# Optimization experiments

Hardware: AMD Instinct MI355X
Metric: run time of the kernel (lower is better)

The kernel has to match this reference:

```python
import jax, jax.numpy as jnp
import numpy as np

B, S, D, H, DM = 2, 2048, 1024, 16, 4
HD = D // H  # head_dim = 64
EPS = 1e-5


def setup_inputs() -> dict:
    key = jax.random.key(0)
    ks = jax.random.split(key, 8)
    s = 0.02
    return {
        "x": jax.random.normal(ks[0], (B, S, D), jnp.float32),
        "wq": jax.random.normal(ks[1], (D, D), jnp.float32) * s,
        "wk": jax.random.normal(ks[2], (D, D), jnp.float32) * s,
        "wv": jax.random.normal(ks[3], (D, D), jnp.float32) * s,
        "wo": jax.random.normal(ks[4], (D, D), jnp.float32) * s,
        "bo": jnp.zeros((D,), jnp.float32),
        "ln1_scale": jnp.ones((D,), jnp.float32),
        "ln1_shift": jnp.zeros((D,), jnp.float32),
        "ln2_scale": jnp.ones((D,), jnp.float32),
        "ln2_shift": jnp.zeros((D,), jnp.float32),
        "w1": jax.random.normal(ks[5], (DM * D, D), jnp.float32) * s,
        "b1": jnp.zeros((DM * D,), jnp.float32),
        "w2": jax.random.normal(ks[6], (D, DM * D), jnp.float32) * s,
        "b2": jnp.zeros((D,), jnp.float32),
    }


def _layernorm(x, scale, shift):
    mean = jnp.mean(x, axis=-1, keepdims=True)
    var = jnp.var(x, axis=-1, keepdims=True)  # unbiased=False
    return scale * (x - mean) * jax.lax.rsqrt(var + EPS) + shift


def _attn(x, wq, wk, wv, wo, bo):
    b, n, d = x.shape
    # torch Linear: y = x @ W.T
    q = (x @ wq.T).reshape(b, n, H, HD).transpose(0, 2, 1, 3)  # [b,h,n,hd]
    k = (x @ wk.T).reshape(b, n, H, HD).transpose(0, 2, 1, 3)
    v = (x @ wv.T).reshape(b, n, H, HD).transpose(0, 2, 1, 3)
    scores = jnp.einsum("bhqd,bhkd->bhqk", q, k)
    causal = jnp.tril(jnp.ones((n, n), bool))
    scores = jnp.where(causal, scores, -jnp.inf)
    w = jax.nn.softmax(scores / np.sqrt(HD).astype(np.float32), axis=-1)
    ctx = jnp.einsum("bhqk,bhkd->bhqd", w, v)
    ctx = ctx.transpose(0, 2, 1, 3).reshape(b, n, d)
    return ctx @ wo.T + bo


def reference(x, wq, wk, wv, wo, bo, ln1_scale, ln1_shift, ln2_scale, ln2_shift, w1, b1, w2, b2):
    h = x + _attn(_layernorm(x, ln1_scale, ln1_shift), wq, wk, wv, wo, bo)
    y = _layernorm(h, ln2_scale, ln2_shift)
    y = jax.nn.relu(y @ w1.T + b1) @ w2.T + b2
    return h + y
```

## Files before the change

kernel.cpp:

```cpp
#include <hip/hip_runtime.h>
#include <hip/hip_bf16.h>

#define DEV __device__ __forceinline__

typedef __attribute__((ext_vector_type(8))) short bf8;
typedef __attribute__((ext_vector_type(4))) float f4;
typedef __attribute__((ext_vector_type(16))) float f16x;

#define GLOAD_LDS(gp, lp) \
  __builtin_amdgcn_global_load_lds( \
      (const __attribute__((address_space(1))) void*)(gp), \
      (__attribute__((address_space(3))) void*)(lp), 16, 0, 0)

DEV unsigned short f2bf(float f) {
  union { __hip_bfloat16 h; unsigned short u; } c;
  c.h = __float2bfloat16(f);
  return c.u;
}
DEV unsigned int pk2(float a, float b) {
  union { __hip_bfloat162 h; unsigned int u; } c;
  c.h = __hip_bfloat162(__float2bfloat16(a), __float2bfloat16(b));
  return c.u;
}

DEV int2 swz_tile(int ob, int nxt, int nyt) {
  const int nb = nxt * nyt;
  const int cpx = nb >> 3;
  const int W = (ob & 7) * cpx + (ob >> 3);
  const int scw = 4 * nyt;
  const int sc = W / scw, rem = W - sc * scw;
  return make_int2(rem >> 2, sc * 4 + (rem & 3));
}

template<bool BIAS, bool RELU, bool OUTBF>
__global__ __launch_bounds__(512, 2) void gemm_bt256(
    const unsigned short* __restrict__ A, const unsigned short* __restrict__ B,
    const float* __restrict__ bias, void* __restrict__ Cout,
    int M, int N, int K, int ldc, int nyt)
{
  __shared__ unsigned short Sl[2][2][256 * 64];
  const int t = threadIdx.x;
  const int w = t >> 6, l = t & 63;
  const int wr = w >> 2, wc = w & 3;
  int2 tt = swz_tile((int)blockIdx.x, N >> 8, nyt);
  const int m0 = tt.x * 256, n0 = tt.y * 256;

  const int srow = w * 32 + (l >> 3);
  const int scol = 8 * ((l & 7) ^ (l >> 3));
  const unsigned short* Ab = A + (size_t)(m0 + srow) * K + scol;
  const unsigned short* Bb = B + (size_t)(n0 + srow) * K + scol;
  const int sdst = w * 2048 + l * 8;

  auto STAGE = [&](int slot, int kt) {
#pragma unroll
    for (int i = 0; i < 4; ++i) {
      GLOAD_LDS(Ab + (size_t)i * 8 * K + kt * 64, &Sl[slot][0][sdst + i * 512]);
      GLOAD_LDS(Bb + (size_t)i * 8 * K + kt * 64, &Sl[slot][1][sdst + i * 512]);
    }
  };

  const f4 fz = {0.f, 0.f, 0.f, 0.f};
  f4 acc[8][4];
#pragma unroll
  for (int i = 0; i < 8; ++i)
#pragma unroll
    for (int j = 0; j < 4; ++j) acc[i][j] = fz;

  const int NT = K >> 6;
  STAGE(0, 0);
  __syncthreads();

  for (int T = 0; T < NT; ++T) {
    if (T + 1 < NT) STAGE((T + 1) & 1, T + 1);
    const int sl = T & 1;
#pragma unroll
    for (int ks = 0; ks < 2; ++ks) {
      const int cb = (ks * 64 + ((l >> 4) * 16)) ^ ((l & 7) << 4);
      bf8 af[8], bg[4];
#pragma unroll
      for (int m = 0; m < 8; ++m)
        af[m] = *(const bf8*)((const char*)&Sl[sl][0][(wr * 128 + m * 16 + (l & 15)) * 64] + cb);
#pragma unroll
      for (int n = 0; n < 4; ++n)
        bg[n] = *(const bf8*)((const char*)&Sl[sl][1][(wc * 64 + n * 16 + (l & 15)) * 64] + cb);
      __builtin_amdgcn_s_setprio(1);
#pragma unroll
      for (int m = 0; m < 8; ++m)
#pragma unroll
        for (int n = 0; n < 4; ++n)
          acc[m][n] = __builtin_amdgcn_mfma_f32_16x16x32_bf16(af[m], bg[n], acc[m][n], 0, 0, 0);
      __builtin_amdgcn_s_setprio(0);
    }
    __syncthreads();
  }

#pragma unroll
  for (int n = 0; n < 4; ++n) {
    const int col = n0 + wc * 64 + n * 16 + (l & 15);
    float bv = 0.f;
    if (BIAS) bv = bias[col];
#pragma unroll
    for (int m = 0; m < 8; ++m) {
#pragma unroll
      for (int r = 0; r < 4; ++r) {
        const int row = m0 + wr * 128 + m * 16 + ((l >> 4) * 4) + r;
        float v = acc[m][n][r] + bv;
        if (RELU) v = fmaxf(v, 0.f);
        if (OUTBF) ((unsigned short*)Cout)[(size_t)row * ldc + col] = f2bf(v);
        else       ((float*)Cout)[(size_t)row * ldc + col] = v;
      }
    }
  }
}

template<bool BIAS, bool RELU, bool RESID, bool OUTBF, bool WRVT>
__global__ __launch_bounds__(256) void gemm_bt64(
    const unsigned short* __restrict__ A, const unsigned short* __restrict__ B,
    const float* __restrict__ bias, const float* __restrict__ resid,
    void* __restrict__ Cout, int M, int N, int K, int ldc,
    unsigned short* __restrict__ vtout)
{
  __shared__ unsigned short Al[2][64 * 64];
  __shared__ unsigned short Bl[2][128 * 64];
  const int t = threadIdx.x;
  const int w = t >> 6, l = t & 63;
  const int wr = w >> 1, wc = w & 1;
  int2 tt = swz_tile((int)blockIdx.x, N >> 7, M >> 6);
  const int m0 = tt.x * 64, n0 = tt.y * 128;

  const int srow = t >> 3;
  const int scol = 8 * ((t & 7) ^ (srow & 7));
  const unsigned short* Ab = A + (size_t)(m0 + srow) * K + scol;
  const unsigned short* Bb = B + (size_t)(n0 + srow) * K + scol;
  const int sdst = srow * 64 + (t & 7) * 8;

  auto STAGE = [&](int slot, int k0) {
#pragma unroll
    for (int i = 0; i < 2; ++i)
      GLOAD_LDS(Ab + (size_t)(i * 32) * K + k0, &Al[slot][sdst + i * 32 * 64]);
#pragma unroll
    for (int i = 0; i < 4; ++i)
      GLOAD_LDS(Bb + (size_t)(i * 32) * K + k0, &Bl[slot][sdst + i * 32 * 64]);
  };

  const f4 fz = {0.f, 0.f, 0.f, 0.f};
  f4 acc[2][4];
#pragma unroll
  for (int i = 0; i < 2; ++i)
#pragma unroll
    for (int j = 0; j < 4; ++j) acc[i][j] = fz;

  const int NT = K >> 6;
  STAGE(0, 0);
  __syncthreads();

  for (int T = 0; T < NT; ++T) {
    if (T + 1 < NT) STAGE((T + 1) & 1, (T + 1) * 64);
    const int sl = T & 1;
#pragma unroll
    for (int ks = 0; ks < 2; ++ks) {
      const int cb = (ks * 64 + ((l >> 4) * 16)) ^ ((l & 7) << 4);
      bf8 af[2], bg[4];
#pragma unroll
      for (int am = 0; am < 2; ++am)
        af[am] = *(const bf8*)((const char*)&Al[sl][(wr * 32 + am * 16 + (l & 15)) * 64] + cb);
#pragma unroll
      for (int bn = 0; bn < 4; ++bn)
        bg[bn] = *(const bf8*)((const char*)&Bl[sl][(wc * 64 + bn * 16 + (l & 15)) * 64] + cb);
      __builtin_amdgcn_s_setprio(1);
#pragma unroll
      for (int am = 0; am < 2; ++am)
#pragma unroll
        for (int bn = 0; bn < 4; ++bn)
          acc[am][bn] = __builtin_amdgcn_mfma_f32_16x16x32_bf16(af[am], bg[bn], acc[am][bn], 0, 0, 0);
      __builtin_amdgcn_s_setprio(0);
    }
    __syncthreads();
  }

#pragma unroll
  for (int bn = 0; bn < 4; ++bn) {
    const int col = n0 + wc * 64 + bn * 16 + (l & 15);
    float bv = 0.f;
    if (BIAS) bv = bias[col];
    const bool isv = WRVT && (col >= 2048);
    const int hh = (col - 2048) >> 6, dd = (col - 2048) & 63;
#pragma unroll
    for (int am = 0; am < 2; ++am) {
#pragma unroll
      for (int r = 0; r < 4; ++r) {
        const int row = m0 + wr * 32 + am * 16 + ((l >> 4) * 4) + r;
        float v = acc[am][bn][r] + bv;
        if (RELU) v = fmaxf(v, 0.f);
        if (RESID) v += resid[(size_t)row * ldc + col];
        if (WRVT && isv) {
          const int bb = row >> 11, ss = row & 2047;
          vtout[((size_t)(bb * 16 + hh) * 64 + dd) * 2048 + ss] = f2bf(v);
        } else if (OUTBF) {
          ((unsigned short*)Cout)[(size_t)row * ldc + col] = f2bf(v);
        } else {
          ((float*)Cout)[(size_t)row * ldc + col] = v;
        }
      }
    }
  }
}

__global__ __launch_bounds__(256, 4) void attn_kernel(
    const unsigned short* __restrict__ qk, const unsigned short* __restrict__ vt,
    unsigned short* __restrict__ ctx)
{
  __shared__ unsigned short SM[2][2][64 * 64];

  const int t = threadIdx.x;
  const int w = t >> 6, l = t & 63;
  const int p = w >> 1;
  const int hi = l >> 5, q = l & 31;
  const int bid = blockIdx.x;
  const int xcd = bid & 7, i = bid >> 3;
  const int g = i >> 5, c = i & 31;
  const int s = (g & 1) ? c : 31 - c;
  const int bh = xcd * 4 + g;
  const int b = bh >> 4, h = bh & 15;
  const int tile = 2 * s + (w & 1);
  const int q0w = tile * 32;
  const int h0 = (s + 2) >> 1;

  const unsigned short* qbase = qk + ((size_t)b * 2048) * 2048 + h * 64;
  const unsigned short* kbase = qbase + 1024;
  const unsigned short* vbase = vt + (size_t)bh * 64 * 2048;
  unsigned short* Kl = &SM[p][0][0];
  unsigned short* Vl = &SM[p][1][0];
  const int tp = t & 127;

  bf8 qf[4];
#pragma unroll
  for (int ksl = 0; ksl < 4; ++ksl)
    qf[ksl] = *(const bf8*)(qbase + (size_t)(q0w + q) * 2048 + ksl * 16 + hi * 8);

  f16x oacc[2];
#pragma unroll
  for (int dn = 0; dn < 2; ++dn)
#pragma unroll
    for (int i2 = 0; i2 < 16; ++i2) oacc[dn][i2] = 0.f;
  float m_ = -1e30f, l_ = 0.f;

  for (int it = 0; it < h0; ++it) {
    const int gi = p ? h0 + it : it;
    const bool act = gi <= s;
    __syncthreads();
    if (act) {
#pragma unroll
      for (int ss = 0; ss < 4; ++ss) {
        const int row = ss * 16 + (tp >> 3);
        const int cb = (tp & 7) * 16;
        const int sb = cb ^ ((row & 7) << 4);
        GLOAD_LDS(kbase + (size_t)(gi * 64 + row) * 2048 + (sb >> 1),
                  &Kl[row * 64 + (cb >> 1)]);
        GLOAD_LDS(vbase + (size_t)row * 2048 + gi * 64 + (sb >> 1),
                  &Vl[row * 64 + (cb >> 1)]);
      }
    }
    __syncthreads();
    if (act) {
      const int kb0 = gi * 64;

      f16x s0, s1;
#pragma unroll
      for (int i2 = 0; i2 < 16; ++i2) { s0[i2] = 0.f; s1[i2] = 0.f; }
      __builtin_amdgcn_s_setprio(1);
#pragma unroll
      for (int ksl = 0; ksl < 4; ++ksl) {
        const int cbq = (ksl * 16 + hi * 8) * 2;
        const int r0 = q, r1 = 32 + q;
        bf8 k0 = *(const bf8*)((const char*)&Kl[r0 * 64] + (cbq ^ ((r0 & 7) << 4)));
        bf8 k1 = *(const bf8*)((const char*)&Kl[r1 * 64] + (cbq ^ ((r1 & 7) << 4)));
        s0 = __builtin_amdgcn_mfma_f32_32x32x16_bf16(k0, qf[ksl], s0, 0, 0, 0);
        s1 = __builtin_amdgcn_mfma_f32_32x32x16_bf16(k1, qf[ksl], s1, 0, 0, 0);
      }
      __builtin_amdgcn_s_setprio(0);

      float pv[32];
      if (gi == s) {
#pragma unroll
        for (int i2 = 0; i2 < 16; ++i2) {
          const int key = kb0 + (i2 & 3) + 8 * (i2 >> 2) + 4 * hi;
          pv[i2]      = (key <= q0w + q)      ? s0[i2] : -1e30f;
          pv[16 + i2] = (key + 32 <= q0w + q) ? s1[i2] : -1e30f;
        }
      } else {
#pragma unroll
        for (int i2 = 0; i2 < 16; ++i2) { pv[i2] = s0[i2]; pv[16 + i2] = s1[i2]; }
      }

      float tm[16];
#pragma unroll
      for (int i2 = 0; i2 < 16; ++i2) tm[i2] = fmaxf(pv[i2], pv[16 + i2]);
#pragma unroll
      for (int st = 8; st >= 1; st >>= 1)
#pragma unroll
        for (int i2 = 0; i2 < 8; ++i2)
          if (i2 < st) tm[i2] = fmaxf(tm[i2], tm[i2 + st]);
      const float pmax = fmaxf(tm[0], __shfl_xor(tm[0], 32));
      if (__any(pmax > m_ + 11.54f)) {
        const float mn = fmaxf(m_, pmax);
        const float alpha = __builtin_amdgcn_exp2f(m_ - mn);
        m_ = mn;
        l_ *= alpha;
#pragma unroll
        for (int dn = 0; dn < 2; ++dn)
#pragma unroll
          for (int i2 = 0; i2 < 16; ++i2) oacc[dn][i2] *= alpha;
      }
#pragma unroll
      for (int i2 = 0; i2 < 32; ++i2) pv[i2] = __builtin_amdgcn_exp2f(pv[i2] - m_);
      float ts[16];
#pragma unroll
      for (int i2 = 0; i2 < 16; ++i2) ts[i2] = pv[i2] + pv[16 + i2];
#pragma unroll
      for (int st = 8; st >= 1; st >>= 1)
#pragma unroll
        for (int i2 = 0; i2 < 8; ++i2)
          if (i2 < st) ts[i2] += ts[i2 + st];
      l_ += ts[0] + __shfl_xor(ts[0], 32);

#pragma unroll
      for (int sg = 0; sg < 2; ++sg) {
        const float* pp = pv + sg * 16;
        unsigned int wds[8];
#pragma unroll
        for (int m = 0; m < 4; ++m) {
          wds[m * 2]     = pk2(pp[4 * m], pp[4 * m + 1]);
          wds[m * 2 + 1] = pk2(pp[4 * m + 2], pp[4 * m + 3]);
        }
#pragma unroll
        for (int kq = 0; kq < 2; ++kq) {
          unsigned int x0 = __shfl_xor((int)(hi ? wds[4 * kq]     : wds[4 * kq + 2]), 32);
          unsigned int x1 = __shfl_xor((int)(hi ? wds[4 * kq + 1] : wds[4 * kq + 3]), 32);
          union { unsigned int u[4]; bf8 v; } pu;
          pu.u[0] = hi ? x0 : wds[4 * kq];
          pu.u[1] = hi ? x1 : wds[4 * kq + 1];
          pu.u[2] = hi ? wds[4 * kq + 2] : x0;
          pu.u[3] = hi ? wds[4 * kq + 3] : x1;
          const bf8 pf = pu.v;
          __builtin_amdgcn_s_setprio(1);
#pragma unroll
          for (int dn = 0; dn < 2; ++dn) {
            const int row = dn * 32 + q;
            const int cb = ((sg * 32 + kq * 16 + hi * 8) * 2) ^ ((row & 7) << 4);
            bf8 vf = *(const bf8*)((const char*)&Vl[row * 64] + cb);
            oacc[dn] = __builtin_amdgcn_mfma_f32_32x32x16_bf16(vf, pf, oacc[dn], 0, 0, 0);
          }
          __builtin_amdgcn_s_setprio(0);
        }
      }
    }
  }

  __syncthreads();
  float* mb = (float*)&SM[0][0][0];
  if (p == 1) {
    float* base = mb + (w & 1) * 2176;
    base[l] = m_;
    base[64 + l] = l_;
#pragma unroll
    for (int dn = 0; dn < 2; ++dn)
#pragma unroll
      for (int i2 = 0; i2 < 16; ++i2)
        base[128 + (dn * 16 + i2) * 64 + l] = oacc[dn][i2];
  }
  __syncthreads();
  if (p == 0) {
    float* base = mb + (w & 1) * 2176;
    const float m2 = base[l], l2 = base[64 + l];
    const float mm = fmaxf(m_, m2);
    const float a0 = __builtin_amdgcn_exp2f(m_ - mm);
    const float a2 = __builtin_amdgcn_exp2f(m2 - mm);
    const float inv = 1.0f / (a0 * l_ + a2 * l2);
    unsigned short* crow = ctx + ((size_t)(b * 2048 + q0w + q)) * 1024 + h * 64;
#pragma unroll
    for (int dn = 0; dn < 2; ++dn)
#pragma unroll
      for (int m = 0; m < 4; ++m) {
        float o0 = a0 * oacc[dn][4 * m]     + a2 * base[128 + (dn * 16 + 4 * m) * 64 + l];
        float o1 = a0 * oacc[dn][4 * m + 1] + a2 * base[128 + (dn * 16 + 4 * m + 1) * 64 + l];
        float o2 = a0 * oacc[dn][4 * m + 2] + a2 * base[128 + (dn * 16 + 4 * m + 2) * 64 + l];
        float o3 = a0 * oacc[dn][4 * m + 3] + a2 * base[128 + (dn * 16 + 4 * m + 3) * 64 + l];
        const int d0 = dn * 32 + 8 * m + 4 * hi;
        *(unsigned int*)(crow + d0)     = pk2(o0 * inv, o1 * inv);
        *(unsigned int*)(crow + d0 + 2) = pk2(o2 * inv, o3 * inv);
      }
  }
}

__global__ __launch_bounds__(256) void ln_kernel(
    const float* __restrict__ x, const float* __restrict__ sc,
    const float* __restrict__ sh, unsigned short* __restrict__ out)
{
  const int row = blockIdx.x, t = threadIdx.x;
  float4 v = ((const float4*)x)[(size_t)row * 256 + t];
  float s = v.x + v.y + v.z + v.w;
  float q = v.x * v.x + v.y * v.y + v.z * v.z + v.w * v.w;
#pragma unroll
  for (int off = 1; off < 64; off <<= 1) {
    s += __shfl_xor(s, off);
    q += __shfl_xor(q, off);
  }
  __shared__ float red[8];
  const int w = t >> 6, l = t & 63;
  if (l == 0) { red[w] = s; red[4 + w] = q; }
  __syncthreads();
  s = red[0] + red[1] + red[2] + red[3];
  q = red[4] + red[5] + red[6] + red[7];
  const float mean = s * (1.0f / 1024.0f);
  const float var = q * (1.0f / 1024.0f) - mean * mean;
  const float rstd = rsqrtf(var + 1e-5f);
  float4 scv = ((const float4*)sc)[t];
  float4 shv = ((const float4*)sh)[t];
  uint2 p;
  p.x = pk2(scv.x * (v.x - mean) * rstd + shv.x, scv.y * (v.y - mean) * rstd + shv.y);
  p.y = pk2(scv.z * (v.z - mean) * rstd + shv.z, scv.w * (v.w - mean) * rstd + shv.w);
  ((uint2*)out)[(size_t)row * 256 + t] = p;
}

__global__ __launch_bounds__(256) void cvt_weights(
    const float* __restrict__ wq, const float* __restrict__ wk,
    const float* __restrict__ wv, const float* __restrict__ wo,
    const float* __restrict__ w1, const float* __restrict__ w2,
    unsigned short* __restrict__ dst)
{
  const int M1 = 1 << 20;
  const int n4 = (12 * M1) / 4;
  const int stride = gridDim.x * 256;
  for (int i4 = blockIdx.x * 256 + threadIdx.x; i4 < n4; i4 += stride) {
    const size_t i = (size_t)i4 * 4;
    const int mi = (int)(i >> 20);
    const float* src;
    size_t off;
    float sc = 1.0f;
    if (mi < 4) {
      src = mi == 0 ? wq : mi == 1 ? wk : mi == 2 ? wv : wo;
      off = i & (size_t)(M1 - 1);
      if (mi == 0) sc = 0.125f * 1.44269504088896f;
    } else if (mi < 8) {
      src = w1; off = i - (size_t)4 * M1;
    } else {
      src = w2; off = i - (size_t)8 * M1;
    }
    float4 v = *(const float4*)(src + off);
    uint2 pq;
    pq.x = pk2(v.x * sc, v.y * sc);
    pq.y = pk2(v.z * sc, v.w * sc);
    ((uint2*)dst)[i4] = pq;
  }
}

extern "C" void kernel_launch(void* const* d_in, const int* in_sizes, int n_in,
                              void* d_out, int out_size, void* d_ws, size_t ws_size,
                              hipStream_t stream)
{
  const float* x    = (const float*)d_in[0];
  const float* wq   = (const float*)d_in[1];
  const float* wk   = (const float*)d_in[2];
  const float* wv   = (const float*)d_in[3];
  const float* wo   = (const float*)d_in[4];
  const float* bo   = (const float*)d_in[5];
  const float* ln1s = (const float*)d_in[6];
  const float* ln1b = (const float*)d_in[7];
  const float* ln2s = (const float*)d_in[8];
  const float* ln2b = (const float*)d_in[9];
  const float* w1   = (const float*)d_in[10];
  const float* b1   = (const float*)d_in[11];
  const float* w2   = (const float*)d_in[12];
  const float* b2   = (const float*)d_in[13];
  float* out = (float*)d_out;

  const int M = 4096;

  unsigned short* ws   = (unsigned short*)d_ws;
  unsigned short* lnb  = ws;
  unsigned short* qkvw = lnb  + (size_t)4096 * 1024;
  unsigned short* wob  = qkvw + (size_t)3072 * 1024;
  unsigned short* w1b  = wob  + (size_t)1024 * 1024;
  unsigned short* w2b  = w1b  + (size_t)4096 * 1024;
  unsigned short* qkb  = w2b  + (size_t)4096 * 1024;
  unsigned short* vtb  = qkb  + (size_t)4096 * 2048;
  unsigned short* ctxb = vtb  + (size_t)32 * 64 * 2048;
  float* hf = (float*)(ctxb + (size_t)4096 * 1024);

  cvt_weights<<<2048, 256, 0, stream>>>(wq, wk, wv, wo, w1, w2, qkvw);

  ln_kernel<<<M, 256, 0, stream>>>(x, ln1s, ln1b, lnb);
  gemm_bt64<false, false, false, true, true><<<1536, 256, 0, stream>>>(
      lnb, qkvw, nullptr, nullptr, qkb, M, 3072, 1024, 2048, vtb);
  attn_kernel<<<1024, 256, 0, stream>>>(qkb, vtb, ctxb);
  gemm_bt64<true, false, true, false, false><<<512, 256, 0, stream>>>(
      ctxb, wob, bo, x, hf, M, 1024, 1024, 1024, nullptr);
  ln_kernel<<<M, 256, 0, stream>>>(hf, ln2s, ln2b, lnb);
  gemm_bt256<true, true, true><<<256, 512, 0, stream>>>(
      lnb, w1b, b1, qkb, M, 4096, 1024, 4096, 16);
  gemm_bt64<true, false, true, false, false><<<512, 256, 0, stream>>>(
      qkb, w2b, b2, hf, out, M, 1024, 4096, 1024, nullptr);
}
```

Measured before the change: 235.0 us.

## Pipeline 256-tile GEMM in quarter stages and use it for QKV projection

Rewrites the 256x256 GEMM main loop so the next K-tile's loads are issued in four quarter-stages, each placed between MFMA sub-blocks with explicit vmcnt waits and raw barriers. The goal is to overlap global-to-LDS traffic with compute instead of staging everything before a single sync. The V-transpose epilogue moves into this kernel, so the QKV projection now runs on the 256-tile kernel (192 blocks) rather than the 64x128 kernel. The hand-counted vmcnt waits are fragile, and 192 blocks may underfill the GPU.

```diff
diff --git a/kernel.cpp b/kernel.cpp
--- a/kernel.cpp
+++ b/kernel.cpp
@@ -11,6 +11,14 @@
   __builtin_amdgcn_global_load_lds( \
       (const __attribute__((address_space(1))) void*)(gp), \
       (__attribute__((address_space(3))) void*)(lp), 16, 0, 0)
+
+#define WAITVM(n) asm volatile("s_waitcnt vmcnt(" #n ")" ::: "memory")
+
+DEV void barrier_raw() {
+  asm volatile("" ::: "memory");
+  __builtin_amdgcn_s_barrier();
+  asm volatile("" ::: "memory");
+}
 
 DEV unsigned short f2bf(float f) {
   union { __hip_bfloat16 h; unsigned short u; } c;
@@ -32,31 +40,49 @@
   return make_int2(rem >> 2, sc * 4 + (rem & 3));
 }
 
-template<bool BIAS, bool RELU, bool OUTBF>
-__global__ __launch_bounds__(512, 2) void gemm_bt256(
+template<bool BIAS, bool RELU, bool OUTBF, bool WRVT>
+__global__ __launch_bounds__(512, 2) void gemm_bt256p(
     const unsigned short* __restrict__ A, const unsigned short* __restrict__ B,
     const float* __restrict__ bias, void* __restrict__ Cout,
-    int M, int N, int K, int ldc, int nyt)
+    int M, int N, int K, int ldc, unsigned short* __restrict__ vtout, int nyt)
 {
-  __shared__ unsigned short Sl[2][2][256 * 64];
+  __shared__ unsigned short Al[2][256 * 64];
+  __shared__ unsigned short Bl[2][256 * 64];
   const int t = threadIdx.x;
   const int w = t >> 6, l = t & 63;
   const int wr = w >> 2, wc = w & 3;
   int2 tt = swz_tile((int)blockIdx.x, N >> 8, nyt);
   const int m0 = tt.x * 256, n0 = tt.y * 256;
 
-  const int srow = w * 32 + (l >> 3);
-  const int scol = 8 * ((l & 7) ^ (l >> 3));
-  const unsigned short* Ab = A + (size_t)(m0 + srow) * K + scol;
-  const unsigned short* Bb = B + (size_t)(n0 + srow) * K + scol;
-  const int sdst = w * 2048 + l * 8;
-
-  auto STAGE = [&](int slot, int kt) {
-#pragma unroll
-    for (int i = 0; i < 4; ++i) {
-      GLOAD_LDS(Ab + (size_t)i * 8 * K + kt * 64, &Sl[slot][0][sdst + i * 512]);
-      GLOAD_LDS(Bb + (size_t)i * 8 * K + kt * 64, &Sl[slot][1][sdst + i * 512]);
-    }
+  const int lr = l >> 3;
+  const int scol = 8 * ((l & 7) ^ lr);
+  const int ldst = (l & 7) * 8;
+
+  auto stage = [&](int half, int slot, int kb) {
+#pragma unroll
+    for (int i = 0; i < 2; ++i) {
+      if (half == 0 || half == 3) {
+        const int row0 = (half == 3 ? 64 : 0) + i * 128 + w * 8;
+        GLOAD_LDS(A + (size_t)(m0 + row0 + lr) * K + kb + scol,
+                  &Al[slot][(row0 + lr) * 64 + ldst]);
+      } else {
+        const int k2 = w + 8 * i;
+        const int row0 = ((k2 >> 2) << 6) + ((k2 & 3) << 3) + (half == 2 ? 32 : 0);
+        GLOAD_LDS(B + (size_t)(n0 + row0 + lr) * K + kb + scol,
+                  &Bl[slot][(row0 + lr) * 64 + ldst]);
+      }
+    }
+  };
+
+  auto rdA = [&](int buf, int am, int ks) {
+    const int row = wr * 128 + am * 16 + (l & 15);
+    const int cb = (ks * 64 + ((l >> 4) * 16)) ^ ((l & 7) << 4);
+    return *(const bf8*)((const char*)&Al[buf][row * 64] + cb);
+  };
+  auto rdB = [&](int buf, int bn, int ks) {
+    const int row = wc * 64 + bn * 16 + (l & 15);
+    const int cb = (ks * 64 + ((l >> 4) * 16)) ^ ((l & 7) << 4);
+    return *(const bf8*)((const char*)&Bl[buf][row * 64] + cb);
   };
 
   const f4 fz = {0.f, 0.f, 0.f, 0.f};
@@ -67,31 +93,78 @@
     for (int j = 0; j < 4; ++j) acc[i][j] = fz;
 
   const int NT = K >> 6;
-  STAGE(0, 0);
-  __syncthreads();
-
-  for (int T = 0; T < NT; ++T) {
-    if (T + 1 < NT) STAGE((T + 1) & 1, T + 1);
-    const int sl = T & 1;
-#pragma unroll
-    for (int ks = 0; ks < 2; ++ks) {
-      const int cb = (ks * 64 + ((l >> 4) * 16)) ^ ((l & 7) << 4);
-      bf8 af[8], bg[4];
-#pragma unroll
-      for (int m = 0; m < 8; ++m)
-        af[m] = *(const bf8*)((const char*)&Sl[sl][0][(wr * 128 + m * 16 + (l & 15)) * 64] + cb);
-#pragma unroll
-      for (int n = 0; n < 4; ++n)
-        bg[n] = *(const bf8*)((const char*)&Sl[sl][1][(wc * 64 + n * 16 + (l & 15)) * 64] + cb);
-      __builtin_amdgcn_s_setprio(1);
-#pragma unroll
-      for (int m = 0; m < 8; ++m)
-#pragma unroll
-        for (int n = 0; n < 4; ++n)
-          acc[m][n] = __builtin_amdgcn_mfma_f32_16x16x32_bf16(af[m], bg[n], acc[m][n], 0, 0, 0);
-      __builtin_amdgcn_s_setprio(0);
-    }
-    __syncthreads();
+  stage(0, 0, 0); stage(1, 0, 0); stage(2, 0, 0); stage(3, 0, 0);
+
+  bf8 af[4][2], bB[4][2];
+
+  for (int kt = 0; kt < NT; ++kt) {
+    const int buf = kt & 1, nb = buf ^ 1;
+    const int kb1 = (kt + 1) * 64;
+    const bool st = (kt + 1 < NT);
+
+    if (st) { stage(0, nb, kb1); WAITVM(6); } else { WAITVM(4); }
+    barrier_raw();
+#pragma unroll
+    for (int am = 0; am < 4; ++am)
+#pragma unroll
+      for (int ks = 0; ks < 2; ++ks) af[am][ks] = rdA(buf, am, ks);
+#pragma unroll
+    for (int bn = 0; bn < 2; ++bn)
+#pragma unroll
+      for (int ks = 0; ks < 2; ++ks) bB[bn][ks] = rdB(buf, bn, ks);
+    __builtin_amdgcn_s_setprio(1);
+#pragma unroll
+    for (int am = 0; am < 4; ++am)
+#pragma unroll
+      for (int bn = 0; bn < 2; ++bn)
+#pragma unroll
+        for (int ks = 0; ks < 2; ++ks)
+          acc[am][bn] = __builtin_amdgcn_mfma_f32_16x16x32_bf16(af[am][ks], bB[bn][ks], acc[am][bn], 0, 0, 0);
+    __builtin_amdgcn_s_setprio(0);
+
+    if (st) { stage(1, nb, kb1); WAITVM(6); } else { WAITVM(2); }
+    barrier_raw();
+#pragma unroll
+    for (int bn = 2; bn < 4; ++bn)
+#pragma unroll
+      for (int ks = 0; ks < 2; ++ks) bB[bn][ks] = rdB(buf, bn, ks);
+    __builtin_amdgcn_s_setprio(1);
+#pragma unroll
+    for (int am = 0; am < 4; ++am)
+#pragma unroll
+      for (int bn = 2; bn < 4; ++bn)
+#pragma unroll
+        for (int ks = 0; ks < 2; ++ks)
+          acc[am][bn] = __builtin_amdgcn_mfma_f32_16x16x32_bf16(af[am][ks], bB[bn][ks], acc[am][bn], 0, 0, 0);
+    __builtin_amdgcn_s_setprio(0);
+
+    if (st) { stage(2, nb, kb1); WAITVM(6); } else { WAITVM(0); }
+    barrier_raw();
+#pragma unroll
+    for (int am = 0; am < 4; ++am)
+#pragma unroll
+      for (int ks = 0; ks < 2; ++ks) af[am][ks] = rdA(buf, am + 4, ks);
+    __builtin_amdgcn_s_setprio(1);
+#pragma unroll
+    for (int am = 0; am < 4; ++am)
+#pragma unroll
+      for (int bn = 0; bn < 2; ++bn)
+#pragma unroll
+        for (int ks = 0; ks < 2; ++ks)
+          acc[am + 4][bn] = __builtin_amdgcn_mfma_f32_16x16x32_bf16(af[am][ks], bB[bn][ks], acc[am + 4][bn], 0, 0, 0);
+    __builtin_amdgcn_s_setprio(0);
+
+    if (st) stage(3, nb, kb1);
+    barrier_raw();
+    __builtin_amdgcn_s_setprio(1);
+#pragma unroll
+    for (int am = 0; am < 4; ++am)
+#pragma unroll
+      for (int bn = 2; bn < 4; ++bn)
+#pragma unroll
+        for (int ks = 0; ks < 2; ++ks)
+          acc[am + 4][bn] = __builtin_amdgcn_mfma_f32_16x16x32_bf16(af[am][ks], bB[bn][ks], acc[am + 4][bn], 0, 0, 0);
+    __builtin_amdgcn_s_setprio(0);
   }
 
 #pragma unroll
@@ -99,6 +172,8 @@
     const int col = n0 + wc * 64 + n * 16 + (l & 15);
     float bv = 0.f;
     if (BIAS) bv = bias[col];
+    const bool isv = WRVT && (col >= 2048);
+    const int hh = (col - 2048) >> 6, dd = (col - 2048) & 63;
 #pragma unroll
     for (int m = 0; m < 8; ++m) {
 #pragma unroll
@@ -106,19 +181,24 @@
         const int row = m0 + wr * 128 + m * 16 + ((l >> 4) * 4) + r;
         float v = acc[m][n][r] + bv;
         if (RELU) v = fmaxf(v, 0.f);
-        if (OUTBF) ((unsigned short*)Cout)[(size_t)row * ldc + col] = f2bf(v);
-        else       ((float*)Cout)[(size_t)row * ldc + col] = v;
-      }
-    }
-  }
-}
-
-template<bool BIAS, bool RELU, bool RESID, bool OUTBF, bool WRVT>
+        if (WRVT && isv) {
+          const int bb = row >> 11, ss = row & 2047;
+          vtout[((size_t)(bb * 16 + hh) * 64 + dd) * 2048 + ss] = f2bf(v);
+        } else if (OUTBF) {
+          ((unsigned short*)Cout)[(size_t)row * ldc + col] = f2bf(v);
+        } else {
+          ((float*)Cout)[(size_t)row * ldc + col] = v;
+        }
+      }
+    }
+  }
+}
+
+template<bool BIAS, bool RELU, bool RESID, bool OUTBF>
 __global__ __launch_bounds__(256) void gemm_bt64(
     const unsigned short* __restrict__ A, const unsigned short* __restrict__ B,
     const float* __restrict__ bias, const float* __restrict__ resid,
-    void* __restrict__ Cout, int M, int N, int K, int ldc,
-    unsigned short* __restrict__ vtout)
+    void* __restrict__ Cout, int M, int N, int K, int ldc)
 {
   __shared__ unsigned short Al[2][64 * 64];
   __shared__ unsigned short Bl[2][128 * 64];
@@ -183,8 +263,6 @@
     const int col = n0 + wc * 64 + bn * 16 + (l & 15);
     float bv = 0.f;
     if (BIAS) bv = bias[col];
-    const bool isv = WRVT && (col >= 2048);
-    const int hh = (col - 2048) >> 6, dd = (col - 2048) & 63;
 #pragma unroll
     for (int am = 0; am < 2; ++am) {
 #pragma unroll
@@ -193,14 +271,8 @@
         float v = acc[am][bn][r] + bv;
         if (RELU) v = fmaxf(v, 0.f);
         if (RESID) v += resid[(size_t)row * ldc + col];
-        if (WRVT && isv) {
-          const int bb = row >> 11, ss = row & 2047;
-          vtout[((size_t)(bb * 16 + hh) * 64 + dd) * 2048 + ss] = f2bf(v);
-        } else if (OUTBF) {
-          ((unsigned short*)Cout)[(size_t)row * ldc + col] = f2bf(v);
-        } else {
-          ((float*)Cout)[(size_t)row * ldc + col] = v;
-        }
+        if (OUTBF) ((unsigned short*)Cout)[(size_t)row * ldc + col] = f2bf(v);
+        else       ((float*)Cout)[(size_t)row * ldc + col] = v;
       }
     }
   }
@@ -491,14 +563,14 @@
   cvt_weights<<<2048, 256, 0, stream>>>(wq, wk, wv, wo, w1, w2, qkvw);
 
   ln_kernel<<<M, 256, 0, stream>>>(x, ln1s, ln1b, lnb);
-  gemm_bt64<false, false, false, true, true><<<1536, 256, 0, stream>>>(
-      lnb, qkvw, nullptr, nullptr, qkb, M, 3072, 1024, 2048, vtb);
+  gemm_bt256p<false, false, true, true><<<192, 512, 0, stream>>>(
+      lnb, qkvw, nullptr, qkb, M, 3072, 1024, 2048, vtb, 16);
   attn_kernel<<<1024, 256, 0, stream>>>(qkb, vtb, ctxb);
-  gemm_bt64<true, false, true, false, false><<<512, 256, 0, stream>>>(
-      ctxb, wob, bo, x, hf, M, 1024, 1024, 1024, nullptr);
+  gemm_bt64<true, false, true, false><<<512, 256, 0, stream>>>(
+      ctxb, wob, bo, x, hf, M, 1024, 1024, 1024);
   ln_kernel<<<M, 256, 0, stream>>>(hf, ln2s, ln2b, lnb);
-  gemm_bt256<true, true, true><<<256, 512, 0, stream>>>(
-      lnb, w1b, b1, qkb, M, 4096, 1024, 4096, 16);
-  gemm_bt64<true, false, true, false, false><<<512, 256, 0, stream>>>(
-      qkb, w2b, b2, hf, out, M, 1024, 4096, 1024, nullptr);
-}
+  gemm_bt256p<true, true, true, false><<<256, 512, 0, stream>>>(
+      lnb, w1b, b1, qkb, M, 4096, 1024, 4096, nullptr, 16);
+  gemm_bt64<true, false, true, false><<<512, 256, 0, stream>>>(
+      qkb, w2b, b2, hf, out, M, 1024, 4096, 1024);
+}
```

Result: slower. 252.2 us (+7.3%).
